# Kernel optimization log

Measured on AMD Instinct MI355X. Metric: run time of the kernel, lower is better.

The kernel has to match this reference:

```python
import jax, jax.numpy as jnp
import numpy as np

N = 50000      # nodes
E = 800000     # edges (before self loops)
H = 2          # attention heads
CH = 64        # per-head hidden channels
IN = 128       # input features
OUT = 64       # output channels
EPS = 1e-5     # batchnorm eps
SLOPE = 0.2    # LeakyReLU negative slope


def _gat_conv(x, src, dst, W, a_src, a_dst, b, concat):
    # x: [N, Fin]; W: [Fin, H*C]; a_src/a_dst: [H, C]
    n = x.shape[0]
    h = (x @ W).reshape(n, H, -1)                       # [N, H, C]
    al_s = (h * a_src).sum(-1)                          # [N, H]
    al_d = (h * a_dst).sum(-1)                          # [N, H]
    e = al_s[src] + al_d[dst]                           # [E, H]
    e = jnp.where(e > 0, e, SLOPE * e)                  # LeakyReLU
    # softmax over edges grouped by destination node
    m = jax.ops.segment_max(e, dst, num_segments=n)
    ex = jnp.exp(e - m[dst])
    den = jax.ops.segment_sum(ex, dst, num_segments=n)
    alpha = ex / (den[dst] + 1e-16)                     # [E, H]
    out = jax.ops.segment_sum(h[src] * alpha[:, :, None], dst, num_segments=n)
    out = out.reshape(n, -1) if concat else out.mean(axis=1)
    return out + b


def _batchnorm(x, g, be):
    mu = x.mean(axis=0)
    var = x.var(axis=0)  # biased, as torch BN uses in training
    return (x - mu) * jax.lax.rsqrt(var + EPS) * g + be


def setup_inputs() -> dict:
    key = jax.random.key(0)
    ks = jax.random.split(key, 18)
    s = 0.1
    inp = {
        "x": jax.random.normal(ks[0], (N, IN), jnp.float32),
        "edge_index": jax.random.randint(ks[1], (2, E), 0, N, jnp.int64),
        # layer 0: IN -> H*CH (concat)
        "W0": jax.random.normal(ks[2], (IN, H * CH), jnp.float32) * s,
        "a_src0": jax.random.normal(ks[3], (H, CH), jnp.float32) * s,
        "a_dst0": jax.random.normal(ks[4], (H, CH), jnp.float32) * s,
        "b0": jnp.zeros((H * CH,), jnp.float32),
        "g0": jnp.ones((H * CH,), jnp.float32),
        "be0": jnp.zeros((H * CH,), jnp.float32),
        # layer 1: H*CH -> H*CH (concat)
        "W1": jax.random.normal(ks[5], (H * CH, H * CH), jnp.float32) * s,
        "a_src1": jax.random.normal(ks[6], (H, CH), jnp.float32) * s,
        "a_dst1": jax.random.normal(ks[7], (H, CH), jnp.float32) * s,
        "b1": jnp.zeros((H * CH,), jnp.float32),
        "g1": jnp.ones((H * CH,), jnp.float32),
        "be1": jnp.zeros((H * CH,), jnp.float32),
        # layer 2: H*CH -> OUT, concat=False (mean over heads)
        "W2": jax.random.normal(ks[8], (H * CH, H * OUT), jnp.float32) * s,
        "a_src2": jax.random.normal(ks[9], (H, OUT), jnp.float32) * s,
        "a_dst2": jax.random.normal(ks[10], (H, OUT), jnp.float32) * s,
        "b2": jnp.zeros((OUT,), jnp.float32),
    }
    return inp


def reference(x, edge_index, W0, a_src0, a_dst0, b0, g0, be0,
              W1, a_src1, a_dst1, b1, g1, be1,
              W2, a_src2, a_dst2, b2):
    # add self loops (PyG GATConv default)
    loop = jnp.arange(N, dtype=edge_index.dtype)
    src = jnp.concatenate([edge_index[0], loop])
    dst = jnp.concatenate([edge_index[1], loop])

    h = _gat_conv(x, src, dst, W0, a_src0, a_dst0, b0, concat=True)
    h = jax.nn.relu(_batchnorm(h, g0, be0))
    # dropout: eval mode (identity)
    h = _gat_conv(h, src, dst, W1, a_src1, a_dst1, b1, concat=True)
    h = jax.nn.relu(_batchnorm(h, g1, be1))
    out = _gat_conv(h, src, dst, W2, a_src2, a_dst2, b2, concat=False)
    return out
```

## Files before the change

kernel.cpp:

```cpp
#include <hip/hip_runtime.h>


#define N_NODES 50000
#define N_EDGES 800000
#define ET (N_EDGES + N_NODES)
#define FDIM 128
#define SLOPE 0.2f
#define BN_EPS 1e-5f
#define SCAN_NB 196

typedef __attribute__((ext_vector_type(8))) short bf16x8;
typedef __attribute__((ext_vector_type(4))) float f32x4;
typedef __attribute__((ext_vector_type(8))) unsigned short u16x8;

__device__ __forceinline__ unsigned short f2bf(float f) {
  unsigned u = __float_as_uint(f);
  u = u + 0x7fffu + ((u >> 16) & 1u);
  return (unsigned short)(u >> 16);
}
__device__ __forceinline__ float bflo(unsigned p) { return __uint_as_float(p << 16); }
__device__ __forceinline__ float bfhi(unsigned p) { return __uint_as_float(p & 0xffff0000u); }


__global__ __launch_bounds__(256) void hist_kernel(const int* __restrict__ dst,
                                                   int* __restrict__ counts) {
  int i = blockIdx.x * 256 + threadIdx.x;
  if (i >= ET) return;
  int d = (i < N_EDGES) ? dst[i] : i - N_EDGES;
  atomicAdd(&counts[d], 1);
}

__global__ __launch_bounds__(256) void scan_blk(const int* __restrict__ counts,
                                                int* __restrict__ rowptr,
                                                int* __restrict__ partials) {
  int i = blockIdx.x * 256 + threadIdx.x;
  int lane = threadIdx.x & 63, wv = threadIdx.x >> 6;
  int c = (i < N_NODES) ? counts[i] : 0;
  int v = c;
#pragma unroll
  for (int off = 1; off < 64; off <<= 1) {
    int u = __shfl_up(v, off);
    if (lane >= off) v += u;
  }
  __shared__ int wsum[4];
  if (lane == 63) wsum[wv] = v;
  __syncthreads();
  int add = 0;
  for (int w = 0; w < wv; ++w) add += wsum[w];
  if (i < N_NODES) rowptr[i] = v - c + add;
  if (threadIdx.x == 255) partials[blockIdx.x] = add + v;
}

__global__ __launch_bounds__(256) void scan_top(int* __restrict__ partials) {
  int t = threadIdx.x;
  int lane = t & 63, wv = t >> 6;
  int c = (t < SCAN_NB) ? partials[t] : 0;
  int v = c;
#pragma unroll
  for (int off = 1; off < 64; off <<= 1) {
    int u = __shfl_up(v, off);
    if (lane >= off) v += u;
  }
  __shared__ int wsum[4];
  if (lane == 63) wsum[wv] = v;
  __syncthreads();
  int add = 0;
  for (int w = 0; w < wv; ++w) add += wsum[w];
  if (t < SCAN_NB) partials[t] = v - c + add;
}

__global__ __launch_bounds__(256) void scan_fin(int* __restrict__ rowptr,
                                                const int* __restrict__ partials,
                                                int* __restrict__ fill) {
  int i = blockIdx.x * 256 + threadIdx.x;
  if (i >= N_NODES) return;
  int v = rowptr[i] + partials[blockIdx.x];
  rowptr[i] = v;
  fill[i] = v;
  if (i == 0) rowptr[N_NODES] = ET;
}

__global__ __launch_bounds__(256) void scatter_kernel(const int* __restrict__ src,
                                                      const int* __restrict__ dst,
                                                      int* __restrict__ fill,
                                                      int* __restrict__ csr_src) {
  int i = blockIdx.x * 256 + threadIdx.x;
  if (i >= ET) return;
  int s, d;
  if (i < N_EDGES) { s = src[i]; d = dst[i]; } else { s = d = i - N_EDGES; }
  int pos = atomicAdd(&fill[d], 1);
  csr_src[pos] = s;
}

__global__ __launch_bounds__(256) void repack_w(const float* __restrict__ W0,
                                                const float* __restrict__ W1,
                                                const float* __restrict__ W2,
                                                unsigned short* __restrict__ Wr) {
  int i = blockIdx.x * 256 + threadIdx.x;
  if (i >= 3 * 16384) return;
  int L = i >> 14, rem = i & 16383;
  int t  = rem >> 11;
  int ks = (rem >> 9) & 3;
  int ln = (rem >> 3) & 63;
  int j  = rem & 7;
  int k   = ks * 32 + (ln >> 4) * 8 + j;
  int col = t * 16 + (ln & 15);
  const float* W = (L == 0) ? W0 : ((L == 1) ? W1 : W2);
  Wr[i] = f2bf(W[k * 128 + col]);
}

__global__ __launch_bounds__(256) void gemm_mfma(const float* __restrict__ Xin,
                                                 const unsigned short* __restrict__ WrL,
                                                 const float* __restrict__ bna,
                                                 const float* __restrict__ g,
                                                 const float* __restrict__ be,
                                                 const float* __restrict__ a_src,
                                                 const float* __restrict__ a_dst,
                                                 unsigned short* __restrict__ Hbf,
                                                 float* __restrict__ als,
                                                 float* __restrict__ ald,
                                                 int doBN) {
  __shared__ unsigned short lds[4][16][128];
  int lane = threadIdx.x & 63;
  int wv   = threadIdx.x >> 6;
  int row0 = blockIdx.x * 64 + wv * 16;
  int gidx = lane & 15;
  int quad = lane >> 4;
  int rA   = row0 + gidx;
  int rAc  = rA < N_NODES ? rA : N_NODES - 1;
  int koff = quad * 8;

  f32x4 acc[8] = {};
#pragma unroll
  for (int ks = 0; ks < 4; ++ks) {
    int cb = ks * 32 + koff;
    const float4* xr = (const float4*)(Xin + (size_t)rAc * FDIM + cb);
    float4 xa = xr[0], xb = xr[1];
    float xv[8] = {xa.x, xa.y, xa.z, xa.w, xb.x, xb.y, xb.z, xb.w};
    bf16x8 afrag;
    if (doBN) {
#pragma unroll
      for (int j = 0; j < 8; ++j) {
        int c = cb + j;
        float mu  = bna[c] * (1.f / N_NODES);
        float var = bna[128 + c] * (1.f / N_NODES) - mu * mu;
        float v = (xv[j] - mu) * rsqrtf(var + BN_EPS) * g[c] + be[c];
        v = v > 0.f ? v : 0.f;
        afrag[j] = (short)f2bf(v);
      }
    } else {
#pragma unroll
      for (int j = 0; j < 8; ++j) afrag[j] = (short)f2bf(xv[j]);
    }
#pragma unroll
    for (int t = 0; t < 8; ++t) {
      bf16x8 bfrag = *(const bf16x8*)(WrL + ((size_t)((t * 4 + ks) * 64 + lane)) * 8);
      acc[t] = __builtin_amdgcn_mfma_f32_16x16x32_bf16(afrag, bfrag, acc[t], 0, 0, 0);
    }
  }

  float vs[2][4] = {}, vd[2][4] = {};
#pragma unroll
  for (int t = 0; t < 8; ++t) {
    int col = t * 16 + gidx;
    float as = a_src[col], ad = a_dst[col];
    int hd = t >> 2;
#pragma unroll
    for (int r = 0; r < 4; ++r) {
      vs[hd][r] = fmaf(acc[t][r], as, vs[hd][r]);
      vd[hd][r] = fmaf(acc[t][r], ad, vd[hd][r]);
    }
  }
#pragma unroll
  for (int off = 1; off < 16; off <<= 1) {
#pragma unroll
    for (int hd = 0; hd < 2; ++hd)
#pragma unroll
      for (int r = 0; r < 4; ++r) {
        vs[hd][r] += __shfl_xor(vs[hd][r], off);
        vd[hd][r] += __shfl_xor(vd[hd][r], off);
      }
  }
  if (gidx == 0) {
#pragma unroll
    for (int r = 0; r < 4; ++r) {
      int row = row0 + quad * 4 + r;
      if (row < N_NODES) {
        als[row * 2 + 0] = vs[0][r]; als[row * 2 + 1] = vs[1][r];
        ald[row * 2 + 0] = vd[0][r]; ald[row * 2 + 1] = vd[1][r];
      }
    }
  }

#pragma unroll
  for (int t = 0; t < 8; ++t)
#pragma unroll
    for (int r = 0; r < 4; ++r)
      lds[wv][quad * 4 + r][t * 16 + gidx] = f2bf(acc[t][r]);
  __syncthreads();
#pragma unroll
  for (int it = 0; it < 4; ++it) {
    int rloc = it * 4 + quad;
    int row = row0 + rloc;
    if (row < N_NODES)
      *(u16x8*)(Hbf + (size_t)row * FDIM + gidx * 8) = *(u16x8*)&lds[wv][rloc][gidx * 8];
  }
}

__global__ __launch_bounds__(256) void fused_agg(const int* __restrict__ rowptr,
                                                 const int* __restrict__ csr_src,
                                                 const unsigned* __restrict__ H2,
                                                 const float* __restrict__ als,
                                                 const float* __restrict__ ald,
                                                 float* __restrict__ A,
                                                 float* __restrict__ out,
                                                 const float* __restrict__ b2,
                                                 float* __restrict__ part,
                                                 int mode) {
  int lane = threadIdx.x & 63;
  bool hi = lane >= 32;
  int n = __builtin_amdgcn_readfirstlane((blockIdx.x * 256 + threadIdx.x) >> 6);
  int beg = rowptr[n], end = rowptr[n + 1];
  float2 adv = ((const float2*)ald)[n];
  float advh = hi ? adv.y : adv.x;

  int b0 = end - 4; if (b0 > beg) b0 = beg; if (b0 < 0) b0 = 0;
  int delta = beg - b0;
  int s0 = csr_src[b0], s1 = csr_src[b0 + 1], s2 = csr_src[b0 + 2], s3 = csr_src[b0 + 3];
  float2 A0 = ((const float2*)als)[s0];
  float2 A1 = ((const float2*)als)[s1];
  float2 A2 = ((const float2*)als)[s2];
  float2 A3 = ((const float2*)als)[s3];
  unsigned h0 = H2[(size_t)s0 * 64 + lane];
  unsigned h1 = H2[(size_t)s1 * 64 + lane];
  unsigned h2 = H2[(size_t)s2 * 64 + lane];
  unsigned h3 = H2[(size_t)s3 * 64 + lane];

  float l = 0.f, ox = 0.f, oy = 0.f;

#define STEP(AL, HH) { \
    float v_ = (hi ? AL.y : AL.x) + advh; \
    v_ = fmaxf(v_, SLOPE * v_); \
    float e_ = __expf(v_); \
    l += e_; \
    ox = fmaf(e_, bflo(HH), ox); \
    oy = fmaf(e_, bfhi(HH), oy); }

  int j = beg;
  for (; j + 4 <= end; j += 4) {
    int p = j + 4;
    int pp = p; if (pp > end - 4) pp = end - 4;
    int t0 = csr_src[pp], t1 = csr_src[pp + 1], t2 = csr_src[pp + 2], t3 = csr_src[pp + 3];
    float2 B0 = ((const float2*)als)[t0];
    float2 B1 = ((const float2*)als)[t1];
    float2 B2 = ((const float2*)als)[t2];
    float2 B3 = ((const float2*)als)[t3];
    unsigned g0 = H2[(size_t)t0 * 64 + lane];
    unsigned g1 = H2[(size_t)t1 * 64 + lane];
    unsigned g2 = H2[(size_t)t2 * 64 + lane];
    unsigned g3 = H2[(size_t)t3 * 64 + lane];

    STEP(A0, h0); STEP(A1, h1); STEP(A2, h2); STEP(A3, h3);

    delta = p - pp;
    A0 = B0; A1 = B1; A2 = B2; A3 = B3;
    h0 = g0; h1 = g1; h2 = g2; h3 = g3;
  }
  int rem = end - j;
  int hi_k = delta + rem;
  if (0 >= delta && 0 < hi_k) STEP(A0, h0);
  if (1 >= delta && 1 < hi_k) STEP(A1, h1);
  if (2 >= delta && 2 < hi_k) STEP(A2, h2);
  if (3 >= delta && 3 < hi_k) STEP(A3, h3);
#undef STEP

  float inv = 1.f / (l + 1e-16f);
  ox *= inv; oy *= inv;

  if (mode == 0) {
    float2 outv = {ox, oy};
    *(float2*)(A + (size_t)n * FDIM + lane * 2) = outv;
    __shared__ float sh[4][4][64];
    int wv = threadIdx.x >> 6;
    sh[wv][0][lane] = ox;
    sh[wv][1][lane] = oy;
    sh[wv][2][lane] = ox * ox;
    sh[wv][3][lane] = oy * oy;
    __syncthreads();
    if (threadIdx.x < 64) {
      int t = threadIdx.x;
      float a0 = 0.f, a1 = 0.f, a2 = 0.f, a3 = 0.f;
#pragma unroll
      for (int w = 0; w < 4; ++w) {
        a0 += sh[w][0][t]; a1 += sh[w][1][t];
        a2 += sh[w][2][t]; a3 += sh[w][3][t];
      }
      float* slot = part + (blockIdx.x & 31) * 256;
      atomicAdd(&slot[2 * t],           a0);
      atomicAdd(&slot[2 * t + 1],       a1);
      atomicAdd(&slot[128 + 2 * t],     a2);
      atomicAdd(&slot[128 + 2 * t + 1], a3);
    }
  } else {
    float px = __shfl_xor(ox, 32);
    float py = __shfl_xor(oy, 32);
    if (lane < 32) {
      int c = lane * 2;
      float2 outv = {0.5f * (ox + px) + b2[c], 0.5f * (oy + py) + b2[c + 1]};
      *(float2*)(out + (size_t)n * 64 + c) = outv;
    }
  }
}

__global__ __launch_bounds__(256) void reduce_bna(const float* __restrict__ part,
                                                  float* __restrict__ bna) {
  int c = threadIdx.x;
  float s = 0.f;
#pragma unroll
  for (int k = 0; k < 32; ++k) s += part[k * 256 + c];
  bna[c] = s;
}

extern "C" void kernel_launch(void* const* d_in, const int* in_sizes, int n_in,
                              void* d_out, int out_size, void* d_ws, size_t ws_size,
                              hipStream_t stream) {
  const float* x  = (const float*)d_in[0];
  const int*   ei = (const int*)d_in[1];
  const int* src = ei;
  const int* dst = ei + N_EDGES;

  const float* W[3]    = {(const float*)d_in[2],  (const float*)d_in[8],  (const float*)d_in[14]};
  const float* asrc[3] = {(const float*)d_in[3],  (const float*)d_in[9],  (const float*)d_in[15]};
  const float* adst[3] = {(const float*)d_in[4],  (const float*)d_in[10], (const float*)d_in[16]};
  const float* g[2]    = {(const float*)d_in[6],  (const float*)d_in[12]};
  const float* be[2]   = {(const float*)d_in[7],  (const float*)d_in[13]};
  const float* b2      = (const float*)d_in[17];

  int*   counts   = (int*)d_ws;
  int*   rowptr   = counts + 50048;
  int*   fill     = rowptr + 50048;
  int*   partials = fill + 50048;
  int*   csr_src  = partials + 256;
  float* bna      = (float*)(csr_src + 850048);
  float* part     = bna + 256;
  float* als      = part + 8192;
  float* ald      = als + 100096;
  unsigned short* Wr  = (unsigned short*)(ald + 100096);
  unsigned short* Hbf = Wr + 3 * 16384;
  float* A        = (float*)(Hbf + (size_t)N_NODES * FDIM);

  hipMemsetAsync(counts, 0, (size_t)N_NODES * sizeof(int), stream);
  hist_kernel<<<(ET + 255) / 256, 256, 0, stream>>>(dst, counts);
  scan_blk<<<SCAN_NB, 256, 0, stream>>>(counts, rowptr, partials);
  scan_top<<<1, 256, 0, stream>>>(partials);
  scan_fin<<<SCAN_NB, 256, 0, stream>>>(rowptr, partials, fill);
  scatter_kernel<<<(ET + 255) / 256, 256, 0, stream>>>(src, dst, fill, csr_src);
  repack_w<<<(3 * 16384 + 255) / 256, 256, 0, stream>>>(W[0], W[1], W[2], Wr);

  const int gemm_grid = (N_NODES + 63) / 64;
  const int agg_grid  = N_NODES * 64 / 256;

  for (int L = 0; L < 3; ++L) {
    const float* fin = (L == 0) ? x : A;
    int doBN = (L > 0);
    const float* gg = doBN ? g[L - 1]  : (const float*)nullptr;
    const float* bb = doBN ? be[L - 1] : (const float*)nullptr;
    gemm_mfma<<<gemm_grid, 256, 0, stream>>>(fin, Wr + (size_t)L * 16384, bna, gg, bb,
                                             asrc[L], adst[L], Hbf, als, ald, doBN);
    if (L < 2)
      hipMemsetAsync(part, 0, 8192 * sizeof(float), stream);
    fused_agg<<<agg_grid, 256, 0, stream>>>(rowptr, csr_src, (const unsigned*)Hbf,
                                            als, ald, A, (float*)d_out, b2, part,
                                            (L == 2) ? 2 : 0);
    if (L < 2)
      reduce_bna<<<1, 256, 0, stream>>>(part, bna);
  }
}
```

Before: 372.3 us.

## Partition CSR build atomics by node range and fold BN stats reduction into GEMM

The histogram and scatter kernels now assign each block a chunk of edges plus one of eight destination-node ranges, and a block only issues atomics for destinations in its range. The intent is to improve locality of atomics and the fill/csr writes, at the price of every edge chunk being read eight times. Separately, the reduce_bna launch is removed: each GEMM block reduces the 32 partial BN sums itself and precomputes per-channel scale/shift in LDS, so the per-element normalization becomes a single fma. This adds redundant reduction work in every GEMM block but saves two launches and per-element rsqrt math.

```diff
diff --git a/kernel.cpp b/kernel.cpp
--- a/kernel.cpp
+++ b/kernel.cpp
@@ -8,6 +8,10 @@
 #define SLOPE 0.2f
 #define BN_EPS 1e-5f
 #define SCAN_NB 196
+#define NRANGE 8
+#define RNODES (N_NODES / NRANGE)
+#define SCAT_SUB 128
+#define SCAT_CH ((ET + SCAT_SUB - 1) / SCAT_SUB)
 
 typedef __attribute__((ext_vector_type(8))) short bf16x8;
 typedef __attribute__((ext_vector_type(4))) float f32x4;
@@ -24,10 +28,15 @@
 
 __global__ __launch_bounds__(256) void hist_kernel(const int* __restrict__ dst,
                                                    int* __restrict__ counts) {
-  int i = blockIdx.x * 256 + threadIdx.x;
-  if (i >= ET) return;
-  int d = (i < N_EDGES) ? dst[i] : i - N_EDGES;
-  atomicAdd(&counts[d], 1);
+  int r = blockIdx.x & (NRANGE - 1);
+  int s = blockIdx.x >> 3;
+  int lo = r * RNODES, hi = lo + RNODES;
+  int e0 = s * SCAT_CH;
+  int e1 = e0 + SCAT_CH; if (e1 > ET) e1 = ET;
+  for (int i = e0 + threadIdx.x; i < e1; i += 256) {
+    int d = (i < N_EDGES) ? dst[i] : i - N_EDGES;
+    if (d >= lo && d < hi) atomicAdd(&counts[d], 1);
+  }
 }
 
 __global__ __launch_bounds__(256) void scan_blk(const int* __restrict__ counts,
@@ -84,12 +93,19 @@
                                                       const int* __restrict__ dst,
                                                       int* __restrict__ fill,
                                                       int* __restrict__ csr_src) {
-  int i = blockIdx.x * 256 + threadIdx.x;
-  if (i >= ET) return;
-  int s, d;
-  if (i < N_EDGES) { s = src[i]; d = dst[i]; } else { s = d = i - N_EDGES; }
-  int pos = atomicAdd(&fill[d], 1);
-  csr_src[pos] = s;
+  int r = blockIdx.x & (NRANGE - 1);
+  int s = blockIdx.x >> 3;
+  int lo = r * RNODES, hi = lo + RNODES;
+  int e0 = s * SCAT_CH;
+  int e1 = e0 + SCAT_CH; if (e1 > ET) e1 = ET;
+  for (int i = e0 + threadIdx.x; i < e1; i += 256) {
+    int d = (i < N_EDGES) ? dst[i] : i - N_EDGES;
+    if (d >= lo && d < hi) {
+      int sv = (i < N_EDGES) ? src[i] : d;
+      int pos = atomicAdd(&fill[d], 1);
+      csr_src[pos] = sv;
+    }
+  }
 }
 
 __global__ __launch_bounds__(256) void repack_w(const float* __restrict__ W0,
@@ -111,7 +127,7 @@
 
 __global__ __launch_bounds__(256) void gemm_mfma(const float* __restrict__ Xin,
                                                  const unsigned short* __restrict__ WrL,
-                                                 const float* __restrict__ bna,
+                                                 const float* __restrict__ part,
                                                  const float* __restrict__ g,
                                                  const float* __restrict__ be,
                                                  const float* __restrict__ a_src,
@@ -121,8 +137,28 @@
                                                  float* __restrict__ ald,
                                                  int doBN) {
   __shared__ unsigned short lds[4][16][128];
+  __shared__ float ls_scale[128], ls_shift[128];
   int lane = threadIdx.x & 63;
   int wv   = threadIdx.x >> 6;
+
+  if (doBN) {
+    int t = threadIdx.x;
+    if (t < 128) {
+      float s = 0.f, q = 0.f;
+#pragma unroll
+      for (int k = 0; k < 32; ++k) {
+        s += part[k * 256 + t];
+        q += part[k * 256 + 128 + t];
+      }
+      float mu  = s * (1.f / N_NODES);
+      float var = q * (1.f / N_NODES) - mu * mu;
+      float sc  = rsqrtf(var + BN_EPS) * g[t];
+      ls_scale[t] = sc;
+      ls_shift[t] = be[t] - mu * sc;
+    }
+    __syncthreads();
+  }
+
   int row0 = blockIdx.x * 64 + wv * 16;
   int gidx = lane & 15;
   int quad = lane >> 4;
@@ -142,9 +178,7 @@
 #pragma unroll
       for (int j = 0; j < 8; ++j) {
         int c = cb + j;
-        float mu  = bna[c] * (1.f / N_NODES);
-        float var = bna[128 + c] * (1.f / N_NODES) - mu * mu;
-        float v = (xv[j] - mu) * rsqrtf(var + BN_EPS) * g[c] + be[c];
+        float v = fmaf(xv[j], ls_scale[c], ls_shift[c]);
         v = v > 0.f ? v : 0.f;
         afrag[j] = (short)f2bf(v);
       }
@@ -312,15 +346,6 @@
   }
 }
 
-__global__ __launch_bounds__(256) void reduce_bna(const float* __restrict__ part,
-                                                  float* __restrict__ bna) {
-  int c = threadIdx.x;
-  float s = 0.f;
-#pragma unroll
-  for (int k = 0; k < 32; ++k) s += part[k * 256 + c];
-  bna[c] = s;
-}
-
 extern "C" void kernel_launch(void* const* d_in, const int* in_sizes, int n_in,
                               void* d_out, int out_size, void* d_ws, size_t ws_size,
                               hipStream_t stream) {
@@ -341,8 +366,7 @@
   int*   fill     = rowptr + 50048;
   int*   partials = fill + 50048;
   int*   csr_src  = partials + 256;
-  float* bna      = (float*)(csr_src + 850048);
-  float* part     = bna + 256;
+  float* part     = (float*)(csr_src + 850048);
   float* als      = part + 8192;
   float* ald      = als + 100096;
   unsigned short* Wr  = (unsigned short*)(ald + 100096);
@@ -350,11 +374,11 @@
   float* A        = (float*)(Hbf + (size_t)N_NODES * FDIM);
 
   hipMemsetAsync(counts, 0, (size_t)N_NODES * sizeof(int), stream);
-  hist_kernel<<<(ET + 255) / 256, 256, 0, stream>>>(dst, counts);
+  hist_kernel<<<NRANGE * SCAT_SUB, 256, 0, stream>>>(dst, counts);
   scan_blk<<<SCAN_NB, 256, 0, stream>>>(counts, rowptr, partials);
   scan_top<<<1, 256, 0, stream>>>(partials);
   scan_fin<<<SCAN_NB, 256, 0, stream>>>(rowptr, partials, fill);
-  scatter_kernel<<<(ET + 255) / 256, 256, 0, stream>>>(src, dst, fill, csr_src);
+  scatter_kernel<<<NRANGE * SCAT_SUB, 256, 0, stream>>>(src, dst, fill, csr_src);
   repack_w<<<(3 * 16384 + 255) / 256, 256, 0, stream>>>(W[0], W[1], W[2], Wr);
 
   const int gemm_grid = (N_NODES + 63) / 64;
@@ -365,14 +389,12 @@
     int doBN = (L > 0);
     const float* gg = doBN ? g[L - 1]  : (const float*)nullptr;
     const float* bb = doBN ? be[L - 1] : (const float*)nullptr;
-    gemm_mfma<<<gemm_grid, 256, 0, stream>>>(fin, Wr + (size_t)L * 16384, bna, gg, bb,
+    gemm_mfma<<<gemm_grid, 256, 0, stream>>>(fin, Wr + (size_t)L * 16384, part, gg, bb,
                                              asrc[L], adst[L], Hbf, als, ald, doBN);
     if (L < 2)
       hipMemsetAsync(part, 0, 8192 * sizeof(float), stream);
     fused_agg<<<agg_grid, 256, 0, stream>>>(rowptr, csr_src, (const unsigned*)Hbf,
                                             als, ald, A, (float*)d_out, b2, part,
                                             (L == 2) ? 2 : 0);
-    if (L < 2)
-      reduce_bna<<<1, 256, 0, stream>>>(part, bna);
-  }
-}
+  }
+}
```

New measurement: 360.7 us. 1.03x faster.
